# Kernel optimization log

Hardware: AMD Instinct MI355X
Metric: run time of the kernel (lower is better)

## Reference

```python
import jax, jax.numpy as jnp
from jax import lax
import numpy as np

# ---- init hyperparameters (from init_kwargs) ----
STRIDE = 1
DP_CHANNELS = 1
ATOM_R = 8
ATOM_C = 8
NUMB_ATOM = 128
T_SC = 3
K = 256
BATCH = 32
IMG = 64


def setup_inputs() -> dict:
    key = jax.random.key(0)
    k1, k2 = jax.random.split(key)
    Y = jax.random.normal(k1, (BATCH, DP_CHANNELS, IMG, IMG), dtype=jnp.float32)
    # ConvTranspose2d weight layout: (numb_atom, dp_channels, atom_c, atom_r)
    W = jax.random.normal(k2, (NUMB_ATOM, DP_CHANNELS, ATOM_C, ATOM_R), dtype=jnp.float32)
    # normalise_weights(): each (i, j) filter divided by its L2 norm
    W = W / jnp.sqrt(jnp.sum(W ** 2, axis=(2, 3), keepdims=True))
    return {"Y": Y, "W_D": W}


def _conv_D(X, W):
    # PyTorch ConvTranspose2d (stride=1, no padding): full convolution with
    # spatially-flipped kernel; W is (in=numb_atom, out=dp_channels, kh, kw).
    kh, kw = W.shape[2], W.shape[3]
    return lax.conv_general_dilated(
        X, jnp.flip(W, (2, 3)), (1, 1),
        [(kh - 1, kh - 1), (kw - 1, kw - 1)],
        dimension_numbers=('NCHW', 'IOHW', 'NCHW'))


def _conv_Dt(R, Wt):
    # PyTorch Conv2d (VALID, stride=1): Wt is (out=numb_atom, in=dp, kh, kw)
    return lax.conv_general_dilated(
        R, Wt, (1, 1), 'VALID', dimension_numbers=('NCHW', 'OIHW', 'NCHW'))


def _hard_threshold_k(X, k):
    # keep the k largest-|.| entries per sample (over flattened C,H,W)
    B = X.shape[0]
    flat = X.reshape(B, -1)
    _, idx = lax.top_k(jnp.abs(flat), k)                      # [B, k]
    vals = jnp.take_along_axis(flat, idx, axis=1)             # [B, k]
    out = jnp.zeros_like(flat).at[jnp.arange(B)[:, None], idx].set(vals)
    return out.reshape(X.shape)


def _linesearch(Y, X, W, Wt, k):
    R = Y - _conv_D(X, W)
    g = _conv_Dt(R, Wt)
    l2_start = jnp.sum(R ** 2)

    def attempt(alpha):
        Xu = _hard_threshold_k(X + alpha * g, k)
        err = jnp.sum((Y - _conv_D(Xu, W)) ** 2)
        return Xu, err

    Xu0, err0 = attempt(jnp.float32(1.0))

    def cond(s):
        _, _, err, count = s
        return (err >= l2_start) & (count <= 15)

    def body(s):
        alpha, _, _, count = s
        alpha = alpha * jnp.float32(0.5)
        Xu, err = attempt(alpha)
        return (alpha, Xu, err, count + 1)

    alpha, Xu, err, _ = lax.while_loop(
        cond, body, (jnp.float32(1.0), Xu0, err0, jnp.int32(0)))
    return Xu, err, alpha


def reference(Y, W_D):
    # D_trans.weight = D.weight.permute(0,1,3,2) -> (numb_atom, dp, atom_r, atom_c)
    Wt = jnp.swapaxes(W_D, 2, 3)
    kh, kw = Wt.shape[2], Wt.shape[3]
    B, _, H, W_sp = Y.shape
    X = jnp.zeros((B, W_D.shape[0], H - kh + 1, W_sp - kw + 1), dtype=Y.dtype)
    for _ in range(T_SC):
        X, _, _ = _linesearch(Y, X, W_D, Wt, K)
    return X
```

## Files before the change

### kernel.cpp

```cpp
#include <hip/hip_runtime.h>
#include <stdint.h>

#define NB   32
#define NCH  128
#define IMG  64
#define IMG2 4096
#define OH   57
#define OHW  3249
#define CHW  415872
#define KTOP 256
#define NATT 17
#define NS   32
#define SCAP 512
#define NCAP 1536
#define NBUCK 8192
#define HSHIFT 18
#define TGT  512
#define RSTRIDE 72
#define NZB  257

typedef unsigned long long ull;

__global__ void k_init(int* support_cnt) {
    if (threadIdx.x < NB) support_cnt[threadIdx.x] = 0;
}

__global__ __launch_bounds__(256) void k_resid(
    const float* __restrict__ Y, const float* __restrict__ W,
    const int* __restrict__ support_cnt, const uint32_t* __restrict__ support_idx,
    const float* __restrict__ support_val, float* __restrict__ Rg, double* __restrict__ l2part,
    uint32_t* __restrict__ hist, int* __restrict__ cand_cnt)
{
    int bx = blockIdx.x, tid = threadIdx.x;
    if (bx >= NB) {
        int zb = bx - NB;
        if (zb < 256) {
            ((uint4*)hist)[zb * 256 + tid] = make_uint4(0u, 0u, 0u, 0u);
        } else {
            ((uint4*)cand_cnt)[tid] = make_uint4(0u, 0u, 0u, 0u);
        }
        return;
    }
    int b = bx;
    __shared__ float Rs[IMG2];
    const float4* Y4 = (const float4*)(Y + b * IMG2);
    float4* R4 = (float4*)Rs;
    for (int i = tid; i < IMG2 / 4; i += 256) R4[i] = Y4[i];
    __syncthreads();
    int n = support_cnt[b];
    for (int task = tid; task < n * 64; task += 256) {
        int i = task >> 6, tap = task & 63, p = tap >> 3, q = tap & 7;
        uint32_t idx = support_idx[b * KTOP + i];
        float val = support_val[b * KTOP + i];
        int c = idx / OHW, rem = idx % OHW, s = rem / OH, t = rem % OH;
        float w = W[c * 64 + p * 8 + q];
        atomicAdd(&Rs[(s + p) * IMG + (t + q)], -val * w);
    }
    __syncthreads();
    double acc = 0.0;
    for (int i = tid; i < IMG2; i += 256) {
        float v = Rs[i];
        Rg[b * IMG2 + i] = v;
        acc += (double)v * (double)v;
    }
    __shared__ double red[256];
    red[tid] = acc; __syncthreads();
    for (int s2 = 128; s2 > 0; s2 >>= 1) { if (tid < s2) red[tid] += red[tid + s2]; __syncthreads(); }
    if (tid == 0) l2part[b] = red[0];
}

__global__ __launch_bounds__(256) void k_conv(
    const float* __restrict__ Rg, const float* __restrict__ W,
    float* __restrict__ g_out, uint32_t* __restrict__ hist)
{
    int b = blockIdx.x, cg0 = blockIdx.y, tid = threadIdx.x;
    __shared__ float Rs[71 * 72];
    __shared__ uint32_t hl[NBUCK];
    for (int i = tid; i < 71 * 72; i += 256) Rs[i] = 0.f;
    for (int i = tid; i < NBUCK; i += 256) hl[i] = 0u;
    __syncthreads();
    const float4* R4 = (const float4*)(Rg + b * IMG2);
    for (int i = tid; i < 1024; i += 256) {
        int row = i >> 4, col4 = (i & 15) * 4;
        *(float4*)&Rs[row * 72 + col4] = R4[i];
    }
    __syncthreads();
    int csub = tid >> 7;
    int tile = tid & 127;
    bool active = tile < 120;
    int tr = active ? tile / 15 : 0;
    int tc = active ? tile % 15 : 0;
    int s0 = tr * 8, t0 = tc * 4;

    for (int sub = 0; sub < 4; ++sub) {
        int c = cg0 * 8 + sub * 2 + csub;
        int c_s = __builtin_amdgcn_readfirstlane(c);
        const float* Wc = W + c_s * 64;

        float acc[8][4];
#pragma unroll
        for (int r = 0; r < 8; ++r)
#pragma unroll
            for (int cc = 0; cc < 4; ++cc) acc[r][cc] = 0.f;

#pragma unroll
        for (int rho = 0; rho < 15; ++rho) {
            float rb[12];
            const float* rp = &Rs[(s0 + rho) * 72 + t0];
            *(float4*)&rb[0] = *(const float4*)rp;
            *(float4*)&rb[4] = *(const float4*)(rp + 4);
            *(float4*)&rb[8] = *(const float4*)(rp + 8);
#pragma unroll
            for (int r = 0; r < 8; ++r) {
                const int p = rho - r;
                if (p >= 0 && p < 8) {
#pragma unroll
                    for (int q = 0; q < 8; ++q) {
                        float wv = Wc[q * 8 + p];
#pragma unroll
                        for (int cc = 0; cc < 4; ++cc)
                            acc[r][cc] = fmaf(rb[cc + q], wv, acc[r][cc]);
                    }
                }
            }
        }
        if (active) {
            float* go = g_out + (size_t)(b * NCH + c) * OHW;
#pragma unroll
            for (int r = 0; r < 8; ++r) {
                int s = s0 + r;
                if (s < OH) {
#pragma unroll
                    for (int cc = 0; cc < 4; ++cc) {
                        int t = t0 + cc;
                        if (t < OH) {
                            float v = acc[r][cc];
                            go[s * OH + t] = v;
                            uint32_t bits = __float_as_uint(v) & 0x7fffffffu;
                            atomicAdd(&hl[bits >> HSHIFT], 1u);
                        }
                    }
                }
            }
        }
    }
    __syncthreads();
    for (int i = tid; i < NBUCK; i += 256) {
        uint32_t v = hl[i];
        if (v) atomicAdd(&hist[b * NBUCK + i], v);
    }
}

__global__ __launch_bounds__(256) void k_thresh(const uint32_t* __restrict__ hist,
                                                uint32_t* __restrict__ thr) {
    int b = blockIdx.x, tid = threadIdx.x;
    uint32_t h[32];
    uint32_t s = 0;
    const uint32_t* hb = hist + b * NBUCK + tid * 32;
#pragma unroll
    for (int k = 0; k < 32; ++k) { h[k] = hb[k]; s += h[k]; }
    __shared__ uint32_t buf[2][256];
    int cur = 0;
    buf[0][tid] = s;
    __syncthreads();
    for (int d = 1; d < 256; d <<= 1) {
        uint32_t v = buf[cur][tid];
        if (tid + d < 256) v += buf[cur][tid + d];
        buf[cur ^ 1][tid] = v;
        cur ^= 1;
        __syncthreads();
    }
    uint32_t sufme = buf[cur][tid];
    uint32_t base  = (tid < 255) ? buf[cur][tid + 1] : 0u;
    if (tid == 0 && buf[cur][0] < TGT) thr[b] = 0u;
    if (base < TGT && sufme >= TGT) {
        uint32_t acc = base; int bk = 0;
#pragma unroll
        for (int k = 31; k >= 0; --k) {
            acc += h[k];
            if (acc >= TGT) { bk = tid * 32 + k; break; }
        }
        thr[b] = (uint32_t)bk << HSHIFT;
    }
}

__global__ __launch_bounds__(256) void k_collect(
    const float* __restrict__ g, const uint32_t* __restrict__ thr,
    int* __restrict__ cand_cnt, uint32_t* __restrict__ cand_idx, float* __restrict__ cand_g)
{
    int b = blockIdx.y;
    int i4 = blockIdx.x * 256 + threadIdx.x;
    if (i4 >= CHW / 4) return;
    int slice = blockIdx.x & (NS - 1);
    uint32_t tb = thr[b];
    float4 v4 = ((const float4*)(g + (size_t)b * CHW))[i4];
    float vv[4] = { v4.x, v4.y, v4.z, v4.w };
#pragma unroll
    for (int k = 0; k < 4; ++k) {
        uint32_t bits = __float_as_uint(vv[k]) & 0x7fffffffu;
        if (bits >= tb) {
            int pos = atomicAdd(&cand_cnt[b * NS + slice], 1);
            if (pos < SCAP) {
                cand_idx[(b * NS + slice) * SCAP + pos] = (uint32_t)(i4 * 4 + k);
                cand_g[(b * NS + slice) * SCAP + pos] = vv[k];
            }
        }
    }
}

__global__ __launch_bounds__(256) void k_suppg(
    const float* __restrict__ g,
    const int* __restrict__ support_cnt, const uint32_t* __restrict__ support_idx,
    const float* __restrict__ support_val,
    const int* __restrict__ cand_cnt, const uint32_t* __restrict__ cand_idx,
    const float* __restrict__ cand_g,
    uint32_t* __restrict__ ns_idx, float* __restrict__ ns_g, uint32_t* __restrict__ ns_pk,
    float* __restrict__ sup_g, uint32_t* __restrict__ sup_pk)
{
    int b = blockIdx.x, tid = threadIdx.x, lane = tid & 63;
    __shared__ uint32_t sidx[KTOP];
    __shared__ float sval[KTOP];
    __shared__ int cnts[NS];
    __shared__ ull ck[NCAP];
    __shared__ float cg_l[NCAP];
    __shared__ int nns_sh;
    int n = support_cnt[b];
    if (tid < NS) cnts[tid] = min(cand_cnt[b * NS + tid], SCAP);
    if (tid == 0) nns_sh = 0;
    if (tid < n) { sidx[tid] = support_idx[b * KTOP + tid]; sval[tid] = support_val[b * KTOP + tid]; }
    __syncthreads();
    (void)sval;
    if (tid < n) {
        uint32_t idx = sidx[tid];
        float gv = g[(size_t)b * CHW + idx];
        sup_g[b * KTOP + tid] = gv;
        int c = idx / OHW, r = idx % OHW, s = r / OH, t = r % OH;
        sup_pk[b * KTOP + tid] = (uint32_t)((c << 12) | (s << 6) | t);
    } else {
        sup_g[b * KTOP + tid] = 0.f;
        sup_pk[b * KTOP + tid] = 0u;
    }
    for (int t0 = tid; t0 < NS * SCAP; t0 += 256) {
        int s = t0 >> 9, j = t0 & (SCAP - 1);
        bool keep = false; uint32_t idx = 0; float gv = 0.f;
        if (j < cnts[s]) {
            idx = cand_idx[(b * NS + s) * SCAP + j];
            gv = cand_g[(b * NS + s) * SCAP + j];
            int lo = 0, hi = n - 1; bool found = false;
            while (lo <= hi) {
                int mid = (lo + hi) >> 1;
                uint32_t m = sidx[mid];
                if (m == idx) { found = true; break; }
                if (m < idx) lo = mid + 1; else hi = mid - 1;
            }
            keep = !found;
        }
        ull mk = __ballot(keep);
        if (mk) {
            int basep = 0;
            if (lane == 0) basep = atomicAdd(&nns_sh, (int)__popcll(mk));
            basep = __shfl(basep, 0, 64);
            if (keep) {
                int p = basep + (int)__popcll(mk & ((1ull << lane) - 1ull));
                if (p < NCAP) {
                    ck[p] = ((ull)(__float_as_uint(gv) & 0x7fffffffu) << 32) | (ull)(uint32_t)(~idx);
                    cg_l[p] = gv;
                }
            }
        }
    }
    __syncthreads();
    int nns = min(nns_sh, NCAP);
    ull myk[6]; int myr[6];
#pragma unroll
    for (int q = 0; q < 6; ++q) { int i = tid + 256 * q; myk[q] = (i < nns) ? ck[i] : 0ull; myr[q] = 0; }
    for (int j = 0; j < nns; ++j) {
        ull kj = ck[j];
#pragma unroll
        for (int q = 0; q < 6; ++q) myr[q] += (kj > myk[q]) ? 1 : 0;
    }
#pragma unroll
    for (int q = 0; q < 6; ++q) {
        int i = tid + 256 * q;
        if (i < nns && myr[q] < KTOP) {
            uint32_t idx = ~(uint32_t)myk[q];
            int r = myr[q];
            ns_idx[b * KTOP + r] = idx;
            ns_g[b * KTOP + r] = cg_l[i];
            int c = idx / OHW, rr = idx % OHW, s = rr / OH, t = rr % OH;
            ns_pk[b * KTOP + r] = (uint32_t)((c << 12) | (s << 6) | t);
        }
    }
}

__global__ __launch_bounds__(256) void k_attempt(
    const float* __restrict__ Y, const float* __restrict__ W,
    const int* __restrict__ support_cnt, const uint32_t* __restrict__ support_idx,
    const float* __restrict__ support_val,
    const float* __restrict__ sup_g, const uint32_t* __restrict__ sup_pk,
    const uint32_t* __restrict__ ns_idx, const float* __restrict__ ns_g,
    const uint32_t* __restrict__ ns_pk,
    uint32_t* __restrict__ sel_idx, float* __restrict__ sel_val, double* __restrict__ err)
{
    int a = blockIdx.x, b = blockIdx.y, tid = threadIdx.x;
    int lane = tid & 63, wid = tid >> 6;
    float alpha = ldexpf(1.f, -a);
    int n = support_cnt[b];

    __shared__ ull ku[512];
    __shared__ uint32_t s_ci[KTOP];
    __shared__ float s_v[KTOP];
    __shared__ uint32_t s_pk[KTOP];
    __shared__ float recon[64 * RSTRIDE];
    __shared__ double redd[4];

    uint32_t nsi = ns_idx[b * KTOP + tid];
    float v_ns = alpha * ns_g[b * KTOP + tid];
    uint32_t pk_ns = ns_pk[b * KTOP + tid];
    ull k_ns = ((ull)(__float_as_uint(v_ns) & 0x7fffffffu) << 32) | (ull)(uint32_t)(~nsi);
    ku[tid] = k_ns;
    uint32_t spi; float v_sup; uint32_t pk_sup;
    if (tid < n) {
        spi = support_idx[b * KTOP + tid];
        v_sup = fmaf(alpha, sup_g[b * KTOP + tid], support_val[b * KTOP + tid]);
        pk_sup = sup_pk[b * KTOP + tid];
    } else {
        spi = (uint32_t)(CHW + tid);
        v_sup = 0.f; pk_sup = 0u;
    }
    ull k_sup = ((ull)(__float_as_uint(v_sup) & 0x7fffffffu) << 32) | (ull)(uint32_t)(~spi);
    ku[256 + tid] = k_sup;
    s_v[tid] = 0.f; s_ci[tid] = 0u; s_pk[tid] = 0u;
    for (int i = tid; i < 64 * RSTRIDE; i += 256) recon[i] = 0.f;
    __syncthreads();

    int c_ns = 0, c_sup = 0;
    for (int j = 0; j < 512; ++j) {
        ull kj = ku[j];
        c_ns += (kj > k_ns) ? 1 : 0;
        c_sup += (kj > k_sup) ? 1 : 0;
    }
    if (c_ns < KTOP) { s_ci[c_ns] = nsi; s_v[c_ns] = v_ns; s_pk[c_ns] = pk_ns; }
    if (c_sup < KTOP) { s_ci[c_sup] = spi; s_v[c_sup] = v_sup; s_pk[c_sup] = pk_sup; }
    __syncthreads();

    sel_idx[((size_t)a * NB + b) * KTOP + tid] = s_ci[tid];
    sel_val[((size_t)a * NB + b) * KTOP + tid] = s_v[tid];

    for (int task = tid; task < KTOP * 64; task += 256) {
        int i = task >> 6, tap = task & 63, p = tap >> 3, q = tap & 7;
        uint32_t pk = s_pk[i];
        float val = s_v[i];
        int c = pk >> 12, s = (pk >> 6) & 63, t = pk & 63;
        atomicAdd(&recon[(s + p) * RSTRIDE + (t + q)], val * W[c * 64 + tap]);
    }
    __syncthreads();

    double accd = 0.0;
    for (int e = tid; e < IMG2; e += 256) {
        float d = Y[b * IMG2 + e] - recon[(e >> 6) * RSTRIDE + (e & 63)];
        accd += (double)d * (double)d;
    }
    for (int d = 32; d > 0; d >>= 1) accd += __shfl_xor(accd, d, 64);
    if (lane == 0) redd[wid] = accd;
    __syncthreads();
    if (tid == 0) err[a * NB + b] = ((redd[0] + redd[1]) + redd[2]) + redd[3];
}

__global__ __launch_bounds__(256) void k_update(
    const double* __restrict__ l2part, const double* __restrict__ err,
    const uint32_t* __restrict__ sel_idx, const float* __restrict__ sel_val,
    int* __restrict__ support_cnt, uint32_t* __restrict__ support_idx, float* __restrict__ support_val)
{
    int b = blockIdx.x, tid = threadIdx.x;
    __shared__ double esum[NATT + 1];
    __shared__ int sel_sh;
    if (tid < NATT) {
        double e = 0.0;
        for (int b2 = 0; b2 < NB; ++b2) e += err[tid * NB + b2];
        esum[tid] = e;
    } else if (tid == NATT) {
        double l2 = 0.0;
        for (int b2 = 0; b2 < NB; ++b2) l2 += l2part[b2];
        esum[NATT] = l2;
    }
    __syncthreads();
    if (tid == 0) {
        double l2 = esum[NATT];
        int sel = NATT - 1;
        for (int a2 = 0; a2 < NATT; ++a2) if (esum[a2] < l2) { sel = a2; break; }
        sel_sh = sel;
    }
    __syncthreads();
    int a = sel_sh;
    __shared__ uint32_t ki[KTOP];
    __shared__ float kv[KTOP];
    ki[tid] = sel_idx[((size_t)a * NB + b) * KTOP + tid];
    kv[tid] = sel_val[((size_t)a * NB + b) * KTOP + tid];
    __syncthreads();
    uint32_t me = ki[tid];
    int rank = 0;
    for (int j = 0; j < KTOP; ++j) rank += (ki[j] < me) ? 1 : 0;
    support_idx[b * KTOP + rank] = me;
    support_val[b * KTOP + rank] = kv[tid];
    if (tid == 0) support_cnt[b] = KTOP;
}

__global__ void k_outzero(float4* __restrict__ out) {
    int i = blockIdx.x * 256 + threadIdx.x;
    if (i < (NB * CHW) / 4) out[i] = make_float4(0.f, 0.f, 0.f, 0.f);
}

__global__ void k_scatter(const uint32_t* __restrict__ support_idx, const float* __restrict__ support_val,
                          float* __restrict__ out) {
    int b = blockIdx.x, tid = threadIdx.x;
    if (tid < KTOP) out[(size_t)b * CHW + support_idx[b * KTOP + tid]] = support_val[b * KTOP + tid];
}

static size_t align256(size_t x) { return (x + 255) & ~(size_t)255; }

extern "C" void kernel_launch(void* const* d_in, const int* in_sizes, int n_in,
                              void* d_out, int out_size, void* d_ws, size_t ws_size,
                              hipStream_t stream)
{
    const float* Y = (const float*)d_in[0];
    const float* W = (const float*)d_in[1];
    float* out = (float*)d_out;

    char* p = (char*)d_ws;
    size_t off = 0;
    auto carve = [&](size_t bytes) { void* r = p + off; off = align256(off + bytes); return r; };
    float*    Rg          = (float*)   carve(NB * IMG2 * sizeof(float));
    uint32_t* hist        = (uint32_t*)carve((size_t)NB * NBUCK * sizeof(uint32_t));
    uint32_t* thr         = (uint32_t*)carve(NB * sizeof(uint32_t));
    int*      cand_cnt    = (int*)     carve(NB * NS * sizeof(int));
    double*   l2part      = (double*)  carve(NB * sizeof(double));
    double*   err         = (double*)  carve(NATT * NB * sizeof(double));
    int*      support_cnt = (int*)     carve(NB * sizeof(int));
    uint32_t* support_idx = (uint32_t*)carve(NB * KTOP * sizeof(uint32_t));
    float*    support_val = (float*)   carve(NB * KTOP * sizeof(float));
    uint32_t* sel_idx     = (uint32_t*)carve((size_t)NATT * NB * KTOP * sizeof(uint32_t));
    float*    sel_val     = (float*)   carve((size_t)NATT * NB * KTOP * sizeof(float));
    uint32_t* cand_idx    = (uint32_t*)carve((size_t)NB * NS * SCAP * sizeof(uint32_t));
    float*    cand_g      = (float*)   carve((size_t)NB * NS * SCAP * sizeof(float));
    uint32_t* ns_idx      = (uint32_t*)carve(NB * KTOP * sizeof(uint32_t));
    float*    ns_gbuf     = (float*)   carve(NB * KTOP * sizeof(float));
    uint32_t* ns_pk       = (uint32_t*)carve(NB * KTOP * sizeof(uint32_t));
    float*    sup_gbuf    = (float*)   carve(NB * KTOP * sizeof(float));
    uint32_t* sup_pk      = (uint32_t*)carve(NB * KTOP * sizeof(uint32_t));
    (void)ws_size; (void)in_sizes; (void)n_in; (void)out_size;

    k_init<<<1, 64, 0, stream>>>(support_cnt);
    for (int t = 0; t < 3; ++t) {
        k_resid<<<NB + NZB, 256, 0, stream>>>(Y, W, support_cnt, support_idx, support_val,
                                              Rg, l2part, hist, cand_cnt);
        k_conv<<<dim3(NB, 16), 256, 0, stream>>>(Rg, W, out, hist);
        k_thresh<<<NB, 256, 0, stream>>>(hist, thr);
        k_collect<<<dim3((CHW / 4 + 255) / 256, NB), 256, 0, stream>>>(out, thr, cand_cnt, cand_idx, cand_g);
        k_suppg<<<NB, 256, 0, stream>>>(out, support_cnt, support_idx, support_val,
                                        cand_cnt, cand_idx, cand_g,
                                        ns_idx, ns_gbuf, ns_pk, sup_gbuf, sup_pk);
        k_attempt<<<dim3(NATT, NB), 256, 0, stream>>>(Y, W, support_cnt, support_idx, support_val,
                                                      sup_gbuf, sup_pk, ns_idx, ns_gbuf, ns_pk,
                                                      sel_idx, sel_val, err);
        k_update<<<NB, 256, 0, stream>>>(l2part, err, sel_idx, sel_val,
                                         support_cnt, support_idx, support_val);
    }
    k_outzero<<<((NB * CHW) / 4 + 255) / 256, 256, 0, stream>>>((float4*)out);
    k_scatter<<<NB, 256, 0, stream>>>(support_idx, support_val, out);
}
```

Measured before the change: 802.8 us.

## Use bitmap support lookup, widen suppg to 1024 threads, split attempt into sel/err

k_suppg now runs 1024 threads per block and tests support membership with a shared-memory bitmap instead of a binary search over the sorted support list. The O(n^2) rank loop is spread over more threads, so each thread holds 2 keys instead of 6. k_attempt is split into k_sel, which ranks and selects and writes packed positions, and k_err, which launches 1024 threads to scatter-accumulate the reconstruction and compute the error. The aim is more parallelism in the latency-bound per-sample kernels, at the cost of an extra launch, a sel_pk round trip through global memory, and a 52KB bitmap that must be cleared on every call.

```diff
diff --git a/kernel.cpp b/kernel.cpp
--- a/kernel.cpp
+++ b/kernel.cpp
@@ -18,6 +18,7 @@
 #define TGT  512
 #define RSTRIDE 72
 #define NZB  257
+#define BMW  12996
 
 typedef unsigned long long ull;
 
@@ -208,52 +209,46 @@
     }
 }
 
-__global__ __launch_bounds__(256) void k_suppg(
+__global__ __launch_bounds__(1024) void k_suppg(
     const float* __restrict__ g,
     const int* __restrict__ support_cnt, const uint32_t* __restrict__ support_idx,
-    const float* __restrict__ support_val,
     const int* __restrict__ cand_cnt, const uint32_t* __restrict__ cand_idx,
     const float* __restrict__ cand_g,
     uint32_t* __restrict__ ns_idx, float* __restrict__ ns_g, uint32_t* __restrict__ ns_pk,
     float* __restrict__ sup_g, uint32_t* __restrict__ sup_pk)
 {
     int b = blockIdx.x, tid = threadIdx.x, lane = tid & 63;
-    __shared__ uint32_t sidx[KTOP];
-    __shared__ float sval[KTOP];
+    __shared__ uint32_t bm[BMW];
     __shared__ int cnts[NS];
     __shared__ ull ck[NCAP];
     __shared__ float cg_l[NCAP];
     __shared__ int nns_sh;
     int n = support_cnt[b];
+    for (int i = tid; i < BMW / 4; i += 1024) ((uint4*)bm)[i] = make_uint4(0u, 0u, 0u, 0u);
     if (tid < NS) cnts[tid] = min(cand_cnt[b * NS + tid], SCAP);
     if (tid == 0) nns_sh = 0;
-    if (tid < n) { sidx[tid] = support_idx[b * KTOP + tid]; sval[tid] = support_val[b * KTOP + tid]; }
-    __syncthreads();
-    (void)sval;
-    if (tid < n) {
-        uint32_t idx = sidx[tid];
-        float gv = g[(size_t)b * CHW + idx];
-        sup_g[b * KTOP + tid] = gv;
-        int c = idx / OHW, r = idx % OHW, s = r / OH, t = r % OH;
-        sup_pk[b * KTOP + tid] = (uint32_t)((c << 12) | (s << 6) | t);
-    } else {
-        sup_g[b * KTOP + tid] = 0.f;
-        sup_pk[b * KTOP + tid] = 0u;
-    }
-    for (int t0 = tid; t0 < NS * SCAP; t0 += 256) {
+    __syncthreads();
+    if (tid < KTOP) {
+        if (tid < n) {
+            uint32_t idx = support_idx[b * KTOP + tid];
+            atomicOr(&bm[idx >> 5], 1u << (idx & 31));
+            float gv = g[(size_t)b * CHW + idx];
+            sup_g[b * KTOP + tid] = gv;
+            int c = idx / OHW, r = idx % OHW, s = r / OH, t = r % OH;
+            sup_pk[b * KTOP + tid] = (uint32_t)((c << 12) | (s << 6) | t);
+        } else {
+            sup_g[b * KTOP + tid] = 0.f;
+            sup_pk[b * KTOP + tid] = 0u;
+        }
+    }
+    __syncthreads();
+    for (int t0 = tid; t0 < NS * SCAP; t0 += 1024) {
         int s = t0 >> 9, j = t0 & (SCAP - 1);
         bool keep = false; uint32_t idx = 0; float gv = 0.f;
         if (j < cnts[s]) {
             idx = cand_idx[(b * NS + s) * SCAP + j];
             gv = cand_g[(b * NS + s) * SCAP + j];
-            int lo = 0, hi = n - 1; bool found = false;
-            while (lo <= hi) {
-                int mid = (lo + hi) >> 1;
-                uint32_t m = sidx[mid];
-                if (m == idx) { found = true; break; }
-                if (m < idx) lo = mid + 1; else hi = mid - 1;
-            }
-            keep = !found;
+            keep = ((bm[idx >> 5] >> (idx & 31)) & 1u) == 0u;
         }
         ull mk = __ballot(keep);
         if (mk) {
@@ -271,17 +266,17 @@
     }
     __syncthreads();
     int nns = min(nns_sh, NCAP);
-    ull myk[6]; int myr[6];
-#pragma unroll
-    for (int q = 0; q < 6; ++q) { int i = tid + 256 * q; myk[q] = (i < nns) ? ck[i] : 0ull; myr[q] = 0; }
+    ull myk[2]; int myr[2];
+#pragma unroll
+    for (int q = 0; q < 2; ++q) { int i = tid + 1024 * q; myk[q] = (i < nns) ? ck[i] : 0ull; myr[q] = 0; }
     for (int j = 0; j < nns; ++j) {
         ull kj = ck[j];
 #pragma unroll
-        for (int q = 0; q < 6; ++q) myr[q] += (kj > myk[q]) ? 1 : 0;
-    }
-#pragma unroll
-    for (int q = 0; q < 6; ++q) {
-        int i = tid + 256 * q;
+        for (int q = 0; q < 2; ++q) myr[q] += (kj > myk[q]) ? 1 : 0;
+    }
+#pragma unroll
+    for (int q = 0; q < 2; ++q) {
+        int i = tid + 1024 * q;
         if (i < nns && myr[q] < KTOP) {
             uint32_t idx = ~(uint32_t)myk[q];
             int r = myr[q];
@@ -293,17 +288,15 @@
     }
 }
 
-__global__ __launch_bounds__(256) void k_attempt(
-    const float* __restrict__ Y, const float* __restrict__ W,
+__global__ __launch_bounds__(256) void k_sel(
     const int* __restrict__ support_cnt, const uint32_t* __restrict__ support_idx,
     const float* __restrict__ support_val,
     const float* __restrict__ sup_g, const uint32_t* __restrict__ sup_pk,
     const uint32_t* __restrict__ ns_idx, const float* __restrict__ ns_g,
     const uint32_t* __restrict__ ns_pk,
-    uint32_t* __restrict__ sel_idx, float* __restrict__ sel_val, double* __restrict__ err)
+    uint32_t* __restrict__ sel_idx, float* __restrict__ sel_val, uint32_t* __restrict__ sel_pk)
 {
     int a = blockIdx.x, b = blockIdx.y, tid = threadIdx.x;
-    int lane = tid & 63, wid = tid >> 6;
     float alpha = ldexpf(1.f, -a);
     int n = support_cnt[b];
 
@@ -311,8 +304,6 @@
     __shared__ uint32_t s_ci[KTOP];
     __shared__ float s_v[KTOP];
     __shared__ uint32_t s_pk[KTOP];
-    __shared__ float recon[64 * RSTRIDE];
-    __shared__ double redd[4];
 
     uint32_t nsi = ns_idx[b * KTOP + tid];
     float v_ns = alpha * ns_g[b * KTOP + tid];
@@ -330,8 +321,6 @@
     }
     ull k_sup = ((ull)(__float_as_uint(v_sup) & 0x7fffffffu) << 32) | (ull)(uint32_t)(~spi);
     ku[256 + tid] = k_sup;
-    s_v[tid] = 0.f; s_ci[tid] = 0u; s_pk[tid] = 0u;
-    for (int i = tid; i < 64 * RSTRIDE; i += 256) recon[i] = 0.f;
     __syncthreads();
 
     int c_ns = 0, c_sup = 0;
@@ -344,10 +333,32 @@
     if (c_sup < KTOP) { s_ci[c_sup] = spi; s_v[c_sup] = v_sup; s_pk[c_sup] = pk_sup; }
     __syncthreads();
 
-    sel_idx[((size_t)a * NB + b) * KTOP + tid] = s_ci[tid];
-    sel_val[((size_t)a * NB + b) * KTOP + tid] = s_v[tid];
-
-    for (int task = tid; task < KTOP * 64; task += 256) {
+    size_t o = ((size_t)a * NB + b) * KTOP + tid;
+    sel_idx[o] = s_ci[tid];
+    sel_val[o] = s_v[tid];
+    sel_pk[o] = s_pk[tid];
+}
+
+__global__ __launch_bounds__(1024) void k_err(
+    const float* __restrict__ Y, const float* __restrict__ W,
+    const float* __restrict__ sel_val, const uint32_t* __restrict__ sel_pk,
+    double* __restrict__ err)
+{
+    int a = blockIdx.x, b = blockIdx.y, tid = threadIdx.x;
+    int lane = tid & 63, wid = tid >> 6;
+    __shared__ float recon[64 * RSTRIDE];
+    __shared__ float s_v[KTOP];
+    __shared__ uint32_t s_pk[KTOP];
+    __shared__ double redd[16];
+
+    for (int i = tid; i < 64 * RSTRIDE; i += 1024) recon[i] = 0.f;
+    if (tid < KTOP) {
+        size_t o = ((size_t)a * NB + b) * KTOP + tid;
+        s_v[tid] = sel_val[o];
+        s_pk[tid] = sel_pk[o];
+    }
+    __syncthreads();
+    for (int task = tid; task < KTOP * 64; task += 1024) {
         int i = task >> 6, tap = task & 63, p = tap >> 3, q = tap & 7;
         uint32_t pk = s_pk[i];
         float val = s_v[i];
@@ -355,16 +366,23 @@
         atomicAdd(&recon[(s + p) * RSTRIDE + (t + q)], val * W[c * 64 + tap]);
     }
     __syncthreads();
-
+    float4 y4 = ((const float4*)(Y + b * IMG2))[tid];
+    int row = tid >> 4, col = (tid & 15) * 4;
+    const float* rr = &recon[row * RSTRIDE + col];
     double accd = 0.0;
-    for (int e = tid; e < IMG2; e += 256) {
-        float d = Y[b * IMG2 + e] - recon[(e >> 6) * RSTRIDE + (e & 63)];
-        accd += (double)d * (double)d;
-    }
+    float d0 = y4.x - rr[0]; accd += (double)d0 * (double)d0;
+    float d1 = y4.y - rr[1]; accd += (double)d1 * (double)d1;
+    float d2 = y4.z - rr[2]; accd += (double)d2 * (double)d2;
+    float d3 = y4.w - rr[3]; accd += (double)d3 * (double)d3;
     for (int d = 32; d > 0; d >>= 1) accd += __shfl_xor(accd, d, 64);
     if (lane == 0) redd[wid] = accd;
     __syncthreads();
-    if (tid == 0) err[a * NB + b] = ((redd[0] + redd[1]) + redd[2]) + redd[3];
+    if (tid == 0) {
+        double e = 0.0;
+#pragma unroll
+        for (int w2 = 0; w2 < 16; ++w2) e += redd[w2];
+        err[a * NB + b] = e;
+    }
 }
 
 __global__ __launch_bounds__(256) void k_update(
@@ -441,6 +459,7 @@
     float*    support_val = (float*)   carve(NB * KTOP * sizeof(float));
     uint32_t* sel_idx     = (uint32_t*)carve((size_t)NATT * NB * KTOP * sizeof(uint32_t));
     float*    sel_val     = (float*)   carve((size_t)NATT * NB * KTOP * sizeof(float));
+    uint32_t* sel_pk      = (uint32_t*)carve((size_t)NATT * NB * KTOP * sizeof(uint32_t));
     uint32_t* cand_idx    = (uint32_t*)carve((size_t)NB * NS * SCAP * sizeof(uint32_t));
     float*    cand_g      = (float*)   carve((size_t)NB * NS * SCAP * sizeof(float));
     uint32_t* ns_idx      = (uint32_t*)carve(NB * KTOP * sizeof(uint32_t));
@@ -457,12 +476,13 @@
         k_conv<<<dim3(NB, 16), 256, 0, stream>>>(Rg, W, out, hist);
         k_thresh<<<NB, 256, 0, stream>>>(hist, thr);
         k_collect<<<dim3((CHW / 4 + 255) / 256, NB), 256, 0, stream>>>(out, thr, cand_cnt, cand_idx, cand_g);
-        k_suppg<<<NB, 256, 0, stream>>>(out, support_cnt, support_idx, support_val,
-                                        cand_cnt, cand_idx, cand_g,
-                                        ns_idx, ns_gbuf, ns_pk, sup_gbuf, sup_pk);
-        k_attempt<<<dim3(NATT, NB), 256, 0, stream>>>(Y, W, support_cnt, support_idx, support_val,
-                                                      sup_gbuf, sup_pk, ns_idx, ns_gbuf, ns_pk,
-                                                      sel_idx, sel_val, err);
+        k_suppg<<<NB, 1024, 0, stream>>>(out, support_cnt, support_idx,
+                                         cand_cnt, cand_idx, cand_g,
+                                         ns_idx, ns_gbuf, ns_pk, sup_gbuf, sup_pk);
+        k_sel<<<dim3(NATT, NB), 256, 0, stream>>>(support_cnt, support_idx, support_val,
+                                                  sup_gbuf, sup_pk, ns_idx, ns_gbuf, ns_pk,
+                                                  sel_idx, sel_val, sel_pk);
+        k_err<<<dim3(NATT, NB), 1024, 0, stream>>>(Y, W, sel_val, sel_pk, err);
         k_update<<<NB, 256, 0, stream>>>(l2part, err, sel_idx, sel_val,
                                          support_cnt, support_idx, support_val);
     }
```

New measurement: 695.6 us. -13.3%, faster.
